# Kernel tuning notes

Measured on AMD Instinct MI355X. Metric: run time of the kernel, lower is better.

Reference implementation:

```python
import jax, jax.numpy as jnp
import numpy as np

N = 8192
D = 10
T_END = 100


def setup_inputs() -> dict:
    key = jax.random.key(0)
    k_t, k_e, k_mu, k_a, k_b = jax.random.split(key, 5)
    # sorted event times in [0, T)
    time_points = jnp.sort(jax.random.uniform(k_t, (N,), dtype=jnp.float32) * T_END)
    event_types = jax.random.randint(k_e, (N,), 0, D)
    mu = jax.random.normal(k_mu, (D,), dtype=jnp.float32)
    log_alpha = jax.random.normal(k_a, (D, D), dtype=jnp.float32)
    log_beta = jax.random.normal(k_b, (D, D), dtype=jnp.float32)
    return {
        "time_points": time_points,
        "event_types": event_types,
        "mu": mu,
        "log_alpha": log_alpha,
        "log_beta": log_beta,
        "T": T_END,
    }


def reference(time_points, event_types, mu, log_alpha, log_beta, T):
    # transform_params: softplus on raw parameters
    mu_s = jax.nn.softplus(mu)          # (D,)
    alpha = jax.nn.softplus(log_alpha)  # (D, D) receiver x trigger
    beta = jax.nn.softplus(log_beta)    # (D, D)

    n = time_points.shape[0]
    # pairwise causal time differences: dt[i, j] = t_i - t_j
    dt = time_points[:, None] - time_points[None, :]          # (N, N)
    a_mat = alpha[event_types[:, None], event_types[None, :]]  # (N, N)
    b_mat = beta[event_types[:, None], event_types[None, :]]   # (N, N)

    # strict lower-triangular causal mask (j < i)
    mask = jnp.tril(jnp.ones((n, n), dtype=bool), k=-1)
    dt_safe = jnp.where(mask, dt, 0.0)  # avoid exp overflow on masked entries
    interaction = jnp.where(mask, a_mat * b_mat * jnp.exp(-b_mat * dt_safe), 0.0)

    intensities = mu_s[event_types] + jnp.sum(interaction, axis=1)  # (N,)
    positive_ll = jnp.sum(jnp.log(intensities))

    # analytic integral of the intensity over [0, T]
    T_f = jnp.float32(T)
    delta_t = (T_f - time_points)[:, None]          # (N, 1)
    rel_alpha = alpha[:, event_types].T             # (N, D)
    rel_beta = beta[:, event_types].T               # (N, D)
    contributions = rel_alpha * (1.0 - jnp.exp(-rel_beta * delta_t))  # (N, D)
    integral = mu_s * T_f + jnp.sum(contributions, axis=0)            # (D,)

    return positive_ll - jnp.sum(integral)
```

## Files before the change

kernel.cpp:

```cpp
#include <hip/hip_runtime.h>


#define N_EV 8192
#define DT 10

static constexpr int OFF_ACC   = 0;
static constexpr int OFF_MU    = 8192;
static constexpr int OFF_ALPHA = 8208;
static constexpr int OFF_BETA  = 8320;
static constexpr int OFF_NBL2  = 8432;
static constexpr int OFF_AB    = 8544;

__device__ __forceinline__ float fast_exp2(float x) {
#if __has_builtin(__builtin_amdgcn_exp2f)
    return __builtin_amdgcn_exp2f(x);
#else
    return exp2f(x);
#endif
}

__device__ __forceinline__ float softplus(float x) {
    return fmaxf(x, 0.0f) + log1pf(expf(-fabsf(x)));
}

__device__ __forceinline__ float read_T(const void* p) {
    float f = *(const float*)p;
    if (f > 0.5f && f < 1.0e9f) return f;
    return (float)(*(const int*)p);
}

__global__ void hawkes_prep(const float* __restrict__ mu,
                            const float* __restrict__ la,
                            const float* __restrict__ lb,
                            float* __restrict__ ws) {
    int t = threadIdx.x;
    if (t < DT * DT) {
        float a = softplus(la[t]);
        float b = softplus(lb[t]);
        ws[OFF_ALPHA + t] = a;
        ws[OFF_BETA  + t] = b;
        ws[OFF_NBL2  + t] = -b * 1.4426950408889634f;
        ws[OFF_AB    + t] = a * b;
    }
    if (t < DT) ws[OFF_MU + t] = softplus(mu[t]);
}

__global__ __launch_bounds__(256) void hawkes_pairs(
        const float* __restrict__ tp, const int* __restrict__ et,
        const float* __restrict__ ws, float* __restrict__ acc) {
    const int ib = blockIdx.y, jb = blockIdx.x;
    if (jb > ib) return;

    __shared__ float2 te_s[256];
    __shared__ float2 tab_s[DT * DT];

    const int tid = threadIdx.x;
    if (tid < DT * DT)
        tab_s[tid] = make_float2(ws[OFF_NBL2 + tid], ws[OFF_AB + tid]);
    const int j0 = jb << 8;
    te_s[tid] = make_float2(tp[j0 + tid], __int_as_float(et[j0 + tid]));
    __syncthreads();

    const int i = (ib << 8) + tid;
    const float ti = tp[i];
    const int rowb = et[i] * DT;
    const int cnt = (ib == jb) ? tid : 256;

    float a0 = 0.0f, a1 = 0.0f;
    int j = 0;
#pragma unroll 2
    for (; j + 2 <= cnt; j += 2) {
        float2 te0 = te_s[j];
        float2 te1 = te_s[j + 1];
        float2 tb0 = tab_s[rowb + __float_as_int(te0.y)];
        float2 tb1 = tab_s[rowb + __float_as_int(te1.y)];
        a0 = fmaf(tb0.y, fast_exp2(tb0.x * (ti - te0.x)), a0);
        a1 = fmaf(tb1.y, fast_exp2(tb1.x * (ti - te1.x)), a1);
    }
    if (j < cnt) {
        float2 te0 = te_s[j];
        float2 tb0 = tab_s[rowb + __float_as_int(te0.y)];
        a0 = fmaf(tb0.y, fast_exp2(tb0.x * (ti - te0.x)), a0);
    }
    const float tot = a0 + a1;
    if (cnt > 0) atomicAdd(&acc[i], tot);
}

__global__ __launch_bounds__(256) void hawkes_finish(
        const float* __restrict__ tp, const int* __restrict__ et,
        const float* __restrict__ ws, const void* __restrict__ Tp,
        float* __restrict__ out) {
    const int i = blockIdx.x * 256 + threadIdx.x;
    const float Tf = read_T(Tp);
    const float ti = tp[i];
    const int e = et[i];

    const float inten = ws[OFF_MU + e] + ws[OFF_ACC + i];
    const float ll = logf(inten);

    const float delta = Tf - ti;
    float contrib = 0.0f;
#pragma unroll
    for (int d = 0; d < DT; ++d) {
        float a  = ws[OFF_ALPHA + d * DT + e];
        float nb = ws[OFF_NBL2  + d * DT + e];
        contrib += a * (1.0f - fast_exp2(nb * delta));
    }
    float val = ll - contrib;

    if (i == 0) {
        float s = 0.0f;
#pragma unroll
        for (int d = 0; d < DT; ++d) s += ws[OFF_MU + d];
        val -= s * Tf;
    }

    for (int o = 32; o > 0; o >>= 1) val += __shfl_down(val, o);
    __shared__ float wsum[4];
    const int lane = threadIdx.x & 63, wv = threadIdx.x >> 6;
    if (lane == 0) wsum[wv] = val;
    __syncthreads();
    if (threadIdx.x == 0)
        atomicAdd(out, wsum[0] + wsum[1] + wsum[2] + wsum[3]);
}

extern "C" void kernel_launch(void* const* d_in, const int* in_sizes, int n_in,
                              void* d_out, int out_size, void* d_ws, size_t ws_size,
                              hipStream_t stream) {
    const float* tp = (const float*)d_in[0];
    const int*   et = (const int*)d_in[1];
    const float* mu = (const float*)d_in[2];
    const float* la = (const float*)d_in[3];
    const float* lb = (const float*)d_in[4];
    const void*  Tp = d_in[5];
    float* out = (float*)d_out;
    float* ws  = (float*)d_ws;

    hipMemsetAsync(ws, 0, N_EV * sizeof(float), stream);
    hipMemsetAsync(out, 0, sizeof(float), stream);

    hawkes_prep<<<1, 128, 0, stream>>>(mu, la, lb, ws);

    dim3 grid(32, 32);
    hawkes_pairs<<<grid, 256, 0, stream>>>(tp, et, ws, ws + OFF_ACC);

    hawkes_finish<<<N_EV / 256, 256, 0, stream>>>(tp, et, ws, Tp, out);
}
```

Measured before the change: 85.85 us.

## Drop prep kernel and memsets; store per-block partials and reduce in one-block finish

Removes the two memsets and the separate parameter-prep kernel by recomputing softplus tables inside each pairs block and inside the finish kernel. The per-row atomicAdd into an accumulator is replaced with plain stores of per-column-block partials into a 32x8192 buffer. A single 1024-thread block then sums the partials, computes the log and integral terms, and writes the output directly with no atomics. This cuts launch and memset overhead and makes the result deterministic, at the cost of a serial single-block finish that reads up to about 1 MB of partials.

New measurement: 122.5 us. +42.7%, slower.

```diff
diff --git a/kernel.cpp b/kernel.cpp
--- a/kernel.cpp
+++ b/kernel.cpp
@@ -3,13 +3,6 @@
 
 #define N_EV 8192
 #define DT 10
-
-static constexpr int OFF_ACC   = 0;
-static constexpr int OFF_MU    = 8192;
-static constexpr int OFF_ALPHA = 8208;
-static constexpr int OFF_BETA  = 8320;
-static constexpr int OFF_NBL2  = 8432;
-static constexpr int OFF_AB    = 8544;
 
 __device__ __forceinline__ float fast_exp2(float x) {
 #if __has_builtin(__builtin_amdgcn_exp2f)
@@ -29,25 +22,10 @@
     return (float)(*(const int*)p);
 }
 
-__global__ void hawkes_prep(const float* __restrict__ mu,
-                            const float* __restrict__ la,
-                            const float* __restrict__ lb,
-                            float* __restrict__ ws) {
-    int t = threadIdx.x;
-    if (t < DT * DT) {
-        float a = softplus(la[t]);
-        float b = softplus(lb[t]);
-        ws[OFF_ALPHA + t] = a;
-        ws[OFF_BETA  + t] = b;
-        ws[OFF_NBL2  + t] = -b * 1.4426950408889634f;
-        ws[OFF_AB    + t] = a * b;
-    }
-    if (t < DT) ws[OFF_MU + t] = softplus(mu[t]);
-}
-
 __global__ __launch_bounds__(256) void hawkes_pairs(
         const float* __restrict__ tp, const int* __restrict__ et,
-        const float* __restrict__ ws, float* __restrict__ acc) {
+        const float* __restrict__ la, const float* __restrict__ lb,
+        float* __restrict__ partial) {
     const int ib = blockIdx.y, jb = blockIdx.x;
     if (jb > ib) return;
 
@@ -55,8 +33,11 @@
     __shared__ float2 tab_s[DT * DT];
 
     const int tid = threadIdx.x;
-    if (tid < DT * DT)
-        tab_s[tid] = make_float2(ws[OFF_NBL2 + tid], ws[OFF_AB + tid]);
+    if (tid < DT * DT) {
+        float a = softplus(la[tid]);
+        float b = softplus(lb[tid]);
+        tab_s[tid] = make_float2(-b * 1.4426950408889634f, a * b);
+    }
     const int j0 = jb << 8;
     te_s[tid] = make_float2(tp[j0 + tid], __int_as_float(et[j0 + tid]));
     __syncthreads();
@@ -82,46 +63,63 @@
         float2 tb0 = tab_s[rowb + __float_as_int(te0.y)];
         a0 = fmaf(tb0.y, fast_exp2(tb0.x * (ti - te0.x)), a0);
     }
-    const float tot = a0 + a1;
-    if (cnt > 0) atomicAdd(&acc[i], tot);
+    partial[(jb << 13) + i] = a0 + a1;
 }
 
-__global__ __launch_bounds__(256) void hawkes_finish(
+__global__ __launch_bounds__(1024) void hawkes_finish(
         const float* __restrict__ tp, const int* __restrict__ et,
-        const float* __restrict__ ws, const void* __restrict__ Tp,
-        float* __restrict__ out) {
-    const int i = blockIdx.x * 256 + threadIdx.x;
+        const float* __restrict__ mu, const float* __restrict__ la,
+        const float* __restrict__ lb, const void* __restrict__ Tp,
+        const float* __restrict__ partial, float* __restrict__ out) {
+    __shared__ float mu_s[DT];
+    __shared__ float alpha_s[DT * DT];
+    __shared__ float nbl2_s[DT * DT];
+
+    const int tid = threadIdx.x;
+    if (tid < DT * DT) {
+        alpha_s[tid] = softplus(la[tid]);
+        nbl2_s[tid]  = -softplus(lb[tid]) * 1.4426950408889634f;
+    }
+    if (tid >= 128 && tid < 128 + DT) mu_s[tid - 128] = softplus(mu[tid - 128]);
+    __syncthreads();
+
     const float Tf = read_T(Tp);
-    const float ti = tp[i];
-    const int e = et[i];
+    float val = 0.0f;
 
-    const float inten = ws[OFF_MU + e] + ws[OFF_ACC + i];
-    const float ll = logf(inten);
+    for (int i = tid; i < N_EV; i += 1024) {
+        const int ib = i >> 8;
+        float acc = 0.0f;
+        for (int jb = 0; jb <= ib; ++jb) acc += partial[(jb << 13) + i];
 
-    const float delta = Tf - ti;
-    float contrib = 0.0f;
+        const int e = et[i];
+        const float inten = mu_s[e] + acc;
+        float v = logf(inten);
+
+        const float delta = Tf - tp[i];
 #pragma unroll
-    for (int d = 0; d < DT; ++d) {
-        float a  = ws[OFF_ALPHA + d * DT + e];
-        float nb = ws[OFF_NBL2  + d * DT + e];
-        contrib += a * (1.0f - fast_exp2(nb * delta));
+        for (int d = 0; d < DT; ++d)
+            v -= alpha_s[d * DT + e] * (1.0f - fast_exp2(nbl2_s[d * DT + e] * delta));
+        val += v;
     }
-    float val = ll - contrib;
 
-    if (i == 0) {
+    if (tid == 0) {
         float s = 0.0f;
 #pragma unroll
-        for (int d = 0; d < DT; ++d) s += ws[OFF_MU + d];
+        for (int d = 0; d < DT; ++d) s += mu_s[d];
         val -= s * Tf;
     }
 
     for (int o = 32; o > 0; o >>= 1) val += __shfl_down(val, o);
-    __shared__ float wsum[4];
-    const int lane = threadIdx.x & 63, wv = threadIdx.x >> 6;
+    __shared__ float wsum[16];
+    const int lane = tid & 63, wv = tid >> 6;
     if (lane == 0) wsum[wv] = val;
     __syncthreads();
-    if (threadIdx.x == 0)
-        atomicAdd(out, wsum[0] + wsum[1] + wsum[2] + wsum[3]);
+    if (tid == 0) {
+        float s = 0.0f;
+#pragma unroll
+        for (int w = 0; w < 16; ++w) s += wsum[w];
+        out[0] = s;
+    }
 }
 
 extern "C" void kernel_launch(void* const* d_in, const int* in_sizes, int n_in,
@@ -136,13 +134,7 @@
     float* out = (float*)d_out;
     float* ws  = (float*)d_ws;
 
-    hipMemsetAsync(ws, 0, N_EV * sizeof(float), stream);
-    hipMemsetAsync(out, 0, sizeof(float), stream);
-
-    hawkes_prep<<<1, 128, 0, stream>>>(mu, la, lb, ws);
-
     dim3 grid(32, 32);
-    hawkes_pairs<<<grid, 256, 0, stream>>>(tp, et, ws, ws + OFF_ACC);
-
-    hawkes_finish<<<N_EV / 256, 256, 0, stream>>>(tp, et, ws, Tp, out);
+    hawkes_pairs<<<grid, 256, 0, stream>>>(tp, et, la, lb, ws);
+    hawkes_finish<<<1, 1024, 0, stream>>>(tp, et, mu, la, lb, Tp, ws, out);
 }
```
